# Kernel tuning notes

Hardware: AMD Instinct MI355X
Metric: run time of the kernel (lower is better)

Reference implementation:

```python
import jax, jax.numpy as jnp
import numpy as np

B, T, IN, H, GAT_HEADS, MHA_HEADS, C = 32, 512, 128, 256, 4, 4, 8
OUT = H // GAT_HEADS          # 64, GAT per-head out_features
HD = H // MHA_HEADS           # 64, MHA head dim
ALPHA = 0.2                   # LeakyReLU slope
EPS = 1e-5                    # LayerNorm eps


def setup_inputs() -> dict:
    key = jax.random.key(0)
    ks = iter(jax.random.split(key, 32))
    def rn(shape, scale=0.05):
        return jax.random.normal(next(ks), shape, dtype=jnp.float32) * scale
    return {
        "x": jax.random.normal(next(ks), (B, T, IN), dtype=jnp.float32),
        # GRU layer 0 / 1 (PyTorch gate order r,z,n)
        "gru_W_ih0": rn((3 * H, IN)), "gru_W_hh0": rn((3 * H, H)),
        "gru_b_ih0": rn((3 * H,)), "gru_b_hh0": rn((3 * H,)),
        "gru_W_ih1": rn((3 * H, H)), "gru_W_hh1": rn((3 * H, H)),
        "gru_b_ih1": rn((3 * H,)), "gru_b_hh1": rn((3 * H,)),
        # GAT: per-head W [H,OUT] and additive attention vector a [2*OUT]
        "gat_W": rn((GAT_HEADS, H, OUT)), "gat_a": rn((GAT_HEADS, 2 * OUT)),
        "ln_g": jnp.ones((H,), jnp.float32), "ln_b": jnp.zeros((H,), jnp.float32),
        # MHA packed in-proj (q,k,v) + out-proj
        "mha_in_w": rn((3 * H, H)), "mha_in_b": rn((3 * H,)),
        "mha_out_w": rn((H, H)), "mha_out_b": rn((H,)),
        "fc1_w": rn((H // 2, H)), "fc1_b": rn((H // 2,)),
        "fc2_w": rn((C, H // 2)), "fc2_b": rn((C,)),
    }


def _gru_layer(x, W_ih, W_hh, b_ih, b_hh):
    # x: [B,T,D] -> hidden states [B,T,H]; PyTorch GRU cell math, gates r,z,n
    xp = jnp.einsum('btd,gd->btg', x, W_ih) + b_ih  # precompute input proj [B,T,3H]
    Hh = W_hh.shape[1]
    def step(h, xp_t):
        g = h @ W_hh.T + b_hh
        xr, xz, xn = jnp.split(xp_t, 3, axis=-1)
        hr, hz, hn = jnp.split(g, 3, axis=-1)
        r = jax.nn.sigmoid(xr + hr)
        z = jax.nn.sigmoid(xz + hz)
        n = jnp.tanh(xn + r * hn)
        h_new = (1.0 - z) * n + z * h
        return h_new, h_new
    h0 = jnp.zeros((x.shape[0], Hh), x.dtype)
    _, hs = jax.lax.scan(step, h0, jnp.swapaxes(xp, 0, 1))
    return jnp.swapaxes(hs, 0, 1)


def _gat_head(h_in, W, a):
    # Additive attention decomposed: e_ij = leakyrelu(a1.h_i + a2.h_j)
    # (exactly equals matmul(cat[h_i,h_j], a) without the [B,T,T,2*OUT] tensor)
    h = h_in @ W                       # [B,T,OUT]
    f_src = h @ a[:OUT]                # [B,T]
    f_dst = h @ a[OUT:]                # [B,T]
    e = jax.nn.leaky_relu(f_src[:, :, None] + f_dst[:, None, :], ALPHA)  # [B,T,T]
    attn = jax.nn.softmax(e, axis=-1)  # dropout is identity in eval mode
    return jnp.einsum('bij,bjd->bid', attn, h)


def _layer_norm(x, g, b):
    mu = x.mean(-1, keepdims=True)
    var = jnp.mean((x - mu) ** 2, -1, keepdims=True)
    return (x - mu) * jax.lax.rsqrt(var + EPS) * g + b


def _forward(x, gru_W_ih0, gru_W_hh0, gru_b_ih0, gru_b_hh0,
             gru_W_ih1, gru_W_hh1, gru_b_ih1, gru_b_hh1,
             gat_W, gat_a, ln_g, ln_b,
             mha_in_w, mha_in_b, mha_out_w, mha_out_b,
             fc1_w, fc1_b, fc2_w, fc2_b):
    g = _gru_layer(x, gru_W_ih0, gru_W_hh0, gru_b_ih0, gru_b_hh0)
    g = _gru_layer(g, gru_W_ih1, gru_W_hh1, gru_b_ih1, gru_b_hh1)  # [B,T,H]
    gat_out = jnp.concatenate([_gat_head(g, gat_W[i], gat_a[i]) for i in range(GAT_HEADS)], axis=-1)
    y = _layer_norm(g + gat_out, ln_g, ln_b)
    # Multihead self-attention (4 heads, eval-mode dropout = identity)
    qkv = y @ mha_in_w.T + mha_in_b
    q, k, v = jnp.split(qkv, 3, axis=-1)
    def split_heads(t):
        return t.reshape(t.shape[0], t.shape[1], MHA_HEADS, HD).transpose(0, 2, 1, 3)
    q, k, v = split_heads(q), split_heads(k), split_heads(v)
    scores = jnp.einsum('bhqd,bhkd->bhqk', q, k) / jnp.sqrt(jnp.float32(HD))
    attn = jax.nn.softmax(scores, axis=-1)
    ctx = jnp.einsum('bhqk,bhkd->bhqd', attn, v)
    ctx = ctx.transpose(0, 2, 1, 3).reshape(y.shape[0], y.shape[1], H)
    attn_out = ctx @ mha_out_w.T + mha_out_b
    pooled = attn_out.mean(axis=1)                    # [B,H]
    hid = jax.nn.relu(pooled @ fc1_w.T + fc1_b)
    return hid @ fc2_w.T + fc2_b                      # [B,C]


def reference(x, gru_W_ih0, gru_W_hh0, gru_b_ih0, gru_b_hh0,
              gru_W_ih1, gru_W_hh1, gru_b_ih1, gru_b_hh1,
              gat_W, gat_a, ln_g, ln_b,
              mha_in_w, mha_in_b, mha_out_w, mha_out_b,
              fc1_w, fc1_b, fc2_w, fc2_b):
    return _forward(x, gru_W_ih0, gru_W_hh0, gru_b_ih0, gru_b_hh0,
                    gru_W_ih1, gru_W_hh1, gru_b_ih1, gru_b_hh1,
                    gat_W, gat_a, ln_g, ln_b,
                    mha_in_w, mha_in_b, mha_out_w, mha_out_b,
                    fc1_w, fc1_b, fc2_w, fc2_b)
```

## Files before the change

kernel.cpp:

```cpp
#include <hip/hip_runtime.h>
#include <math.h>

#define BB 32
#define TT 512
#define INF_ 128
#define HH 256
#define H3 768
#define NHEADS 4
#define HDIM 64

typedef _Float16 half_t;
typedef half_t half2_t __attribute__((ext_vector_type(2)));
typedef half_t half4_t __attribute__((ext_vector_type(4)));
typedef half_t f16x8 __attribute__((ext_vector_type(8)));
typedef float f32x4 __attribute__((ext_vector_type(4)));

#if defined(__has_builtin)
#if __has_builtin(__builtin_amdgcn_fdot2)
#define FDOT2(a, b, c) __builtin_amdgcn_fdot2((a), (b), (c), false)
#endif
#endif
#ifndef FDOT2
#define FDOT2(a, b, c) fmaf((float)(a).x, (float)(b).x, fmaf((float)(a).y, (float)(b).y, (c)))
#endif

#define BCH(x) __builtin_bit_cast(half2_t, x)
#define PKH(a, b) __builtin_bit_cast(unsigned, half2_t{(half_t)(a), (half_t)(b)})

__device__ __forceinline__ float wsum(float v) {
#pragma unroll
  for (int o = 32; o > 0; o >>= 1) v += __shfl_xor(v, o, 64);
  return v;
}
__device__ __forceinline__ float wmax(float v) {
#pragma unroll
  for (int o = 32; o > 0; o >>= 1) v = fmaxf(v, __shfl_xor(v, o, 64));
  return v;
}

__global__ void castk(const float* __restrict__ s, half_t* __restrict__ d, int n) {
  int i = (blockIdx.x * 256 + threadIdx.x) * 4;
  if (i < n) {
    float4 v = *(const float4*)(s + i);
    half4_t o = {(half_t)v.x, (half_t)v.y, (half_t)v.z, (half_t)v.w};
    *(half4_t*)(d + i) = o;
  }
}

__global__ __launch_bounds__(256) void gemm_f16(
    const half_t* __restrict__ A, const half_t* __restrict__ B,
    const float* __restrict__ bias, float* __restrict__ C,
    int M, int N, int K) {
  __shared__ __align__(16) half_t As[128][40];
  __shared__ __align__(16) half_t Bs[64][40];
  const int tid = threadIdx.x;
  const int wave = tid >> 6, lane = tid & 63;
  const int m0 = blockIdx.y * 128, n0 = blockIdx.x * 64;
  const int mrow = lane & 15, quad = lane >> 4;
  f32x4 acc00 = {0.f, 0.f, 0.f, 0.f}, acc01 = acc00, acc02 = acc00, acc03 = acc00;
  f32x4 acc10 = acc00, acc11 = acc00, acc12 = acc00, acc13 = acc00;
  for (int k0 = 0; k0 < K; k0 += 32) {
    __syncthreads();
#pragma unroll
    for (int u = 0; u < 2; ++u) {
      int idx = tid + u * 256;
      int row = idx >> 2, seg = idx & 3;
      *(f16x8*)&As[row][seg * 8] =
          *(const f16x8*)&A[(size_t)(m0 + row) * K + k0 + seg * 8];
    }
    {
      int row = tid >> 2, seg = tid & 3;
      *(f16x8*)&Bs[row][seg * 8] =
          *(const f16x8*)&B[(size_t)(n0 + row) * K + k0 + seg * 8];
    }
    __syncthreads();
    f16x8 af0 = *(const f16x8*)&As[wave * 32 + mrow][quad * 8];
    f16x8 af1 = *(const f16x8*)&As[wave * 32 + 16 + mrow][quad * 8];
    f16x8 bf0 = *(const f16x8*)&Bs[mrow][quad * 8];
    f16x8 bf1 = *(const f16x8*)&Bs[16 + mrow][quad * 8];
    f16x8 bf2 = *(const f16x8*)&Bs[32 + mrow][quad * 8];
    f16x8 bf3 = *(const f16x8*)&Bs[48 + mrow][quad * 8];
    acc00 = __builtin_amdgcn_mfma_f32_16x16x32_f16(af0, bf0, acc00, 0, 0, 0);
    acc01 = __builtin_amdgcn_mfma_f32_16x16x32_f16(af0, bf1, acc01, 0, 0, 0);
    acc02 = __builtin_amdgcn_mfma_f32_16x16x32_f16(af0, bf2, acc02, 0, 0, 0);
    acc03 = __builtin_amdgcn_mfma_f32_16x16x32_f16(af0, bf3, acc03, 0, 0, 0);
    acc10 = __builtin_amdgcn_mfma_f32_16x16x32_f16(af1, bf0, acc10, 0, 0, 0);
    acc11 = __builtin_amdgcn_mfma_f32_16x16x32_f16(af1, bf1, acc11, 0, 0, 0);
    acc12 = __builtin_amdgcn_mfma_f32_16x16x32_f16(af1, bf2, acc12, 0, 0, 0);
    acc13 = __builtin_amdgcn_mfma_f32_16x16x32_f16(af1, bf3, acc13, 0, 0, 0);
  }
  float bv0 = bias ? bias[n0 + mrow] : 0.f;
  float bv1 = bias ? bias[n0 + 16 + mrow] : 0.f;
  float bv2 = bias ? bias[n0 + 32 + mrow] : 0.f;
  float bv3 = bias ? bias[n0 + 48 + mrow] : 0.f;
  const int rb = m0 + wave * 32 + quad * 4;
#pragma unroll
  for (int r = 0; r < 4; ++r) {
    float* c0 = C + (size_t)(rb + r) * N + n0;
    c0[mrow] = acc00[r] + bv0;
    c0[16 + mrow] = acc01[r] + bv1;
    c0[32 + mrow] = acc02[r] + bv2;
    c0[48 + mrow] = acc03[r] + bv3;
    float* c1 = C + (size_t)(rb + 16 + r) * N + n0;
    c1[mrow] = acc10[r] + bv0;
    c1[16 + mrow] = acc11[r] + bv1;
    c1[32 + mrow] = acc12[r] + bv2;
    c1[48 + mrow] = acc13[r] + bv3;
  }
}

#define LDW(g, p, a, b, i)                             \
  {                                                    \
    float4 v = (p)[i];                                 \
    g##a = half2_t{(half_t)v.x, (half_t)v.y};          \
    g##b = half2_t{(half_t)v.z, (half_t)v.w};          \
  }
#define LDW28(g, p)                                                        \
  LDW(g, p, 0, 1, 0) LDW(g, p, 2, 3, 1) LDW(g, p, 4, 5, 2)                 \
  LDW(g, p, 6, 7, 3) LDW(g, p, 8, 9, 4) LDW(g, p, 10, 11, 5)               \
  LDW(g, p, 12, 13, 6) LDW(g, p, 14, 15, 7) LDW(g, p, 16, 17, 8)           \
  LDW(g, p, 18, 19, 9) LDW(g, p, 20, 21, 10) LDW(g, p, 22, 23, 11)         \
  LDW(g, p, 24, 25, 12) LDW(g, p, 26, 27, 13) LDW(g, p, 28, 29, 14)        \
  LDW(g, p, 30, 31, 15) LDW(g, p, 32, 33, 16) LDW(g, p, 34, 35, 17)        \
  LDW(g, p, 36, 37, 18) LDW(g, p, 38, 39, 19) LDW(g, p, 40, 41, 20)        \
  LDW(g, p, 42, 43, 21) LDW(g, p, 44, 45, 22) LDW(g, p, 46, 47, 23)        \
  LDW(g, p, 48, 49, 24) LDW(g, p, 50, 51, 25) LDW(g, p, 52, 53, 26)        \
  LDW(g, p, 54, 55, 27)

#define DECL56(g)                                                          \
  half2_t g##0, g##1, g##2, g##3, g##4, g##5, g##6, g##7, g##8, g##9,      \
      g##10, g##11, g##12, g##13, g##14, g##15, g##16, g##17, g##18,       \
      g##19, g##20, g##21, g##22, g##23, g##24, g##25, g##26, g##27,       \
      g##28, g##29, g##30, g##31, g##32, g##33, g##34, g##35, g##36,       \
      g##37, g##38, g##39, g##40, g##41, g##42, g##43, g##44, g##45,       \
      g##46, g##47, g##48, g##49, g##50, g##51, g##52, g##53, g##54, g##55;

#define CHA(c8, a0, a1, a2, a3)                                            \
  {                                                                        \
    float4 v = hp4[c8];                                                    \
    uint4 nv = WSq[((c8)-1) * 512 + tid];                                  \
    half2_t t0 = __builtin_bit_cast(half2_t, v.x);                         \
    half2_t t1 = __builtin_bit_cast(half2_t, v.y);                         \
    half2_t t2 = __builtin_bit_cast(half2_t, v.z);                         \
    half2_t t3 = __builtin_bit_cast(half2_t, v.w);                         \
    ar = FDOT2(wr##a0, t0, ar); az = FDOT2(wz##a0, t0, az); an = FDOT2(BCH(nv.x), t0, an); \
    ar = FDOT2(wr##a1, t1, ar); az = FDOT2(wz##a1, t1, az); an = FDOT2(BCH(nv.y), t1, an); \
    ar = FDOT2(wr##a2, t2, ar); az = FDOT2(wz##a2, t2, az); an = FDOT2(BCH(nv.z), t2, an); \
    ar = FDOT2(wr##a3, t3, ar); az = FDOT2(wz##a3, t3, az); an = FDOT2(BCH(nv.w), t3, an); \
  }

#define CHB(c8)                                                            \
  {                                                                        \
    float4 v = hp4[c8];                                                    \
    uint4 nv = WSq[((c8)-1) * 512 + tid];                                  \
    uint4 rv = WSq[(15 + ((c8)-14)) * 512 + tid];                          \
    uint4 zv = WSq[(17 + ((c8)-14)) * 512 + tid];                          \
    half2_t t0 = __builtin_bit_cast(half2_t, v.x);                         \
    half2_t t1 = __builtin_bit_cast(half2_t, v.y);                         \
    half2_t t2 = __builtin_bit_cast(half2_t, v.z);                         \
    half2_t t3 = __builtin_bit_cast(half2_t, v.w);                         \
    ar = FDOT2(BCH(rv.x), t0, ar); az = FDOT2(BCH(zv.x), t0, az); an = FDOT2(BCH(nv.x), t0, an); \
    ar = FDOT2(BCH(rv.y), t1, ar); az = FDOT2(BCH(zv.y), t1, az); an = FDOT2(BCH(nv.y), t1, an); \
    ar = FDOT2(BCH(rv.z), t2, ar); az = FDOT2(BCH(zv.z), t2, az); an = FDOT2(BCH(nv.z), t2, an); \
    ar = FDOT2(BCH(rv.w), t3, ar); az = FDOT2(BCH(zv.w), t3, az); an = FDOT2(BCH(nv.w), t3, an); \
  }

__device__ __forceinline__ uint4 pk8(const float* p) {
  float4 a = *(const float4*)p;
  float4 b = *(const float4*)(p + 4);
  return uint4{PKH(a.x, a.y), PKH(a.z, a.w), PKH(b.x, b.y), PKH(b.z, b.w)};
}

__global__ __launch_bounds__(512) void gru_layer(
    const float* __restrict__ xp, const float* __restrict__ Whh,
    const float* __restrict__ bhh, float* __restrict__ out,
    half_t* __restrict__ out16) {
  __shared__ __align__(16) uint4 WSq[19 * 512];
  __shared__ __align__(16) half_t hs[2][2][144];
  const int tid = threadIdx.x;
  const int kh = tid & 1, j = tid >> 1;
  const int b = blockIdx.x;
  const bool wf32 = (out != nullptr);
  DECL56(wr)
  DECL56(wz)
  half2_t wn0, wn1, wn2, wn3;
  {
    const float4* pr = (const float4*)(Whh + (size_t)j * HH + kh * 128);
    const float4* pz = (const float4*)(Whh + (size_t)(HH + j) * HH + kh * 128);
    const float4* pn = (const float4*)(Whh + (size_t)(2 * HH + j) * HH + kh * 128);
    LDW28(wr, pr)
    LDW28(wz, pz)
    LDW(wn, pn, 0, 1, 0)
    LDW(wn, pn, 2, 3, 1)
  }
  {
    const float* rowN = Whh + (size_t)(2 * HH + j) * HH + kh * 128;
    const float* rowR = Whh + (size_t)j * HH + kh * 128;
    const float* rowZ = Whh + (size_t)(HH + j) * HH + kh * 128;
#pragma unroll
    for (int sg = 0; sg < 15; ++sg) WSq[sg * 512 + tid] = pk8(rowN + 8 + 8 * sg);
#pragma unroll
    for (int sg = 0; sg < 2; ++sg) WSq[(15 + sg) * 512 + tid] = pk8(rowR + 112 + 8 * sg);
#pragma unroll
    for (int sg = 0; sg < 2; ++sg) WSq[(17 + sg) * 512 + tid] = pk8(rowZ + 112 + 8 * sg);
  }
  const float br = bhh[j], bz = bhh[HH + j], bn = bhh[2 * HH + j];
  for (int i = tid; i < 288; i += 512) ((unsigned*)hs)[i] = 0u;
  __syncthreads();
  float hprev = 0.f;
  const float* xrow = xp + (size_t)b * TT * H3;
  float* orow = out + (size_t)b * TT * HH;
  half_t* orow16 = out16 + (size_t)b * TT * HH;
  for (int t = 0; t < TT; ++t) {
    float xr = xrow[j], xz = xrow[HH + j], xn = xrow[2 * HH + j];
    const float4* hp4 = (const float4*)&hs[t & 1][kh][0];
    float ar = 0.f, az = 0.f, an = 0.f;
    {
      float4 v = hp4[0];
      half2_t t0 = __builtin_bit_cast(half2_t, v.x);
      half2_t t1 = __builtin_bit_cast(half2_t, v.y);
      half2_t t2 = __builtin_bit_cast(half2_t, v.z);
      half2_t t3 = __builtin_bit_cast(half2_t, v.w);
      ar = FDOT2(wr0, t0, ar); az = FDOT2(wz0, t0, az); an = FDOT2(wn0, t0, an);
      ar = FDOT2(wr1, t1, ar); az = FDOT2(wz1, t1, az); an = FDOT2(wn1, t1, an);
      ar = FDOT2(wr2, t2, ar); az = FDOT2(wz2, t2, az); an = FDOT2(wn2, t2, an);
      ar = FDOT2(wr3, t3, ar); az = FDOT2(wz3, t3, az); an = FDOT2(wn3, t3, an);
    }
    CHA(1, 4, 5, 6, 7)
    CHA(2, 8, 9, 10, 11)
    CHA(3, 12, 13, 14, 15)
    CHA(4, 16, 17, 18, 19)
    CHA(5, 20, 21, 22, 23)
    CHA(6, 24, 25, 26, 27)
    CHA(7, 28, 29, 30, 31)
    CHA(8, 32, 33, 34, 35)
    CHA(9, 36, 37, 38, 39)
    CHA(10, 40, 41, 42, 43)
    CHA(11, 44, 45, 46, 47)
    CHA(12, 48, 49, 50, 51)
    CHA(13, 52, 53, 54, 55)
    CHB(14)
    CHB(15)
    ar += __shfl_xor(ar, 1);
    az += __shfl_xor(az, 1);
    an += __shfl_xor(an, 1);
    float rg = 1.f / (1.f + __expf(-(xr + ar + br)));
    float zg = 1.f / (1.f + __expf(-(xz + az + bz)));
    float ng = 2.f / (1.f + __expf(-2.f * (xn + rg * (an + bn)))) - 1.f;
    float hnew = (1.f - zg) * ng + zg * hprev;
    hprev = hnew;
    float hpart = __shfl_xor(hnew, 2);
    if ((tid & 3) == 0) {
      half2_t pk;
      pk.x = (half_t)hnew;
      pk.y = (half_t)hpart;
      *(half2_t*)&hs[(t + 1) & 1][j >> 7][j & 127] = pk;
    }
    if (kh == 0) {
      orow16[j] = (half_t)hnew;
      if (wf32) orow[j] = hnew;
    }
    __syncthreads();
    xrow += H3;
    orow += HH;
    orow16 += HH;
  }
}

__global__ void gat_wt(const float* __restrict__ W, half_t* __restrict__ Wt) {
  int idx = blockIdx.x * 256 + threadIdx.x;
  int col = idx >> 8, k = idx & 255;
  Wt[idx] = (half_t)W[((size_t)((col >> 6) * HH + k)) * HDIM + (col & 63)];
}

__global__ void gat_fsd(const float* __restrict__ hgat, const float* __restrict__ a,
                        float* __restrict__ fsrc, float* __restrict__ fdst) {
  int b = blockIdx.x, hd = blockIdx.y, t = threadIdx.x;
  const float* hp = hgat + ((size_t)(b * TT + t)) * HH + hd * HDIM;
  const float* ap = a + hd * 2 * HDIM;
  float fs = 0.f, fd = 0.f;
#pragma unroll 4
  for (int d = 0; d < HDIM; ++d) {
    float hv = hp[d];
    fs += hv * ap[d];
    fd += hv * ap[HDIM + d];
  }
  fsrc[(b * NHEADS + hd) * TT + t] = fs;
  fdst[(b * NHEADS + hd) * TT + t] = fd;
}

__global__ __launch_bounds__(256) void gat_attn(
    const float* __restrict__ hgat, const float* __restrict__ fsrc,
    const float* __restrict__ fdst, float* __restrict__ out) {
  __shared__ __align__(16) float Ht[128][64];
  __shared__ __align__(16) float fd[128];
  __shared__ __align__(16) float pq[4][128][8];
  const int tid = threadIdx.x, wave = tid >> 6, lane = tid & 63;
  const int hd = blockIdx.y, b = blockIdx.z;
  const int i0 = blockIdx.x * 32 + wave * 8;
  const float* fs = fsrc + (size_t)(b * NHEADS + hd) * TT;
  const float* fdp = fdst + (size_t)(b * NHEADS + hd) * TT;
  float m[8], l[8], acc[8], fi[8];
#pragma unroll
  for (int q = 0; q < 8; ++q) { m[q] = -1e30f; l[q] = 0.f; acc[q] = 0.f; fi[q] = fs[i0 + q]; }
  for (int jt = 0; jt < TT; jt += 128) {
#pragma unroll
    for (int u = 0; u < 8; ++u) {
      int idx = tid + u * 256;
      int jj = idx >> 4, dq = (idx & 15) * 4;
      *(float4*)&Ht[jj][dq] =
          *(const float4*)&hgat[((size_t)(b * TT + jt + jj)) * HH + hd * HDIM + dq];
    }
    if (tid < 128) fd[tid] = fdp[jt + tid];
    __syncthreads();
#pragma unroll
    for (int q = 0; q < 8; ++q) {
      float e0 = fi[q] + fd[lane];      e0 = (e0 > 0.f) ? e0 : 0.2f * e0;
      float e1 = fi[q] + fd[lane + 64]; e1 = (e1 > 0.f) ? e1 : 0.2f * e1;
      float mn = fmaxf(m[q], wmax(fmaxf(e0, e1)));
      float corr = __expf(m[q] - mn);
      float p0 = __expf(e0 - mn), p1 = __expf(e1 - mn);
      l[q] = l[q] * corr + wsum(p0 + p1);
      m[q] = mn;
      acc[q] *= corr;
      pq[wave][lane][q] = p0;
      pq[wave][lane + 64][q] = p1;
    }
#pragma unroll 4
    for (int jj = 0; jj < 128; ++jj) {
      float4 pa = *(const float4*)&pq[wave][jj][0];
      float4 pb = *(const float4*)&pq[wave][jj][4];
      float hv = Ht[jj][lane];
      acc[0] += pa.x * hv; acc[1] += pa.y * hv; acc[2] += pa.z * hv; acc[3] += pa.w * hv;
      acc[4] += pb.x * hv; acc[5] += pb.y * hv; acc[6] += pb.z * hv; acc[7] += pb.w * hv;
    }
    __syncthreads();
  }
#pragma unroll
  for (int q = 0; q < 8; ++q)
    out[((size_t)(b * TT + i0 + q)) * HH + hd * HDIM + lane] = acc[q] / l[q];
}

__global__ __launch_bounds__(256) void ln_res(
    const float* __restrict__ g, const float* __restrict__ gat,
    const float* __restrict__ gamma, const float* __restrict__ beta,
    half_t* __restrict__ y16) {
  int wave = threadIdx.x >> 6, lane = threadIdx.x & 63;
  size_t n = (size_t)blockIdx.x * 4 + wave;
  float4 v = ((const float4*)(g + n * HH))[lane];
  float4 w = ((const float4*)(gat + n * HH))[lane];
  v.x += w.x; v.y += w.y; v.z += w.z; v.w += w.w;
  float mu = wsum(v.x + v.y + v.z + v.w) * (1.f / 256.f);
  float dx = v.x - mu, dy = v.y - mu, dz = v.z - mu, dw = v.w - mu;
  float var = wsum(dx * dx + dy * dy + dz * dz + dw * dw) * (1.f / 256.f);
  float rstd = rsqrtf(var + 1e-5f);
  float4 gm = ((const float4*)gamma)[lane];
  float4 bt = ((const float4*)beta)[lane];
  half4_t o = {(half_t)(dx * rstd * gm.x + bt.x), (half_t)(dy * rstd * gm.y + bt.y),
               (half_t)(dz * rstd * gm.z + bt.z), (half_t)(dw * rstd * gm.w + bt.w)};
  ((half4_t*)(y16 + n * HH))[lane] = o;
}

__global__ __launch_bounds__(256) void mha_attn(const float* __restrict__ qkv,
                                                half_t* __restrict__ ctx16) {
  __shared__ __align__(16) float KV[8320];
  __shared__ __align__(16) float qq[4][64][8];
  __shared__ __align__(16) float pq[4][128][8];
  const int tid = threadIdx.x, wave = tid >> 6, lane = tid & 63;
  const int hd = blockIdx.y, b = blockIdx.z;
  const int i0 = blockIdx.x * 32 + wave * 8;
#pragma unroll
  for (int q = 0; q < 8; ++q)
    qq[wave][lane][q] = qkv[((size_t)(b * TT + i0 + q)) * H3 + hd * HDIM + lane];
  float m[8], l[8], acc[8];
#pragma unroll
  for (int q = 0; q < 8; ++q) { m[q] = -1e30f; l[q] = 0.f; acc[q] = 0.f; }
  for (int jt = 0; jt < TT; jt += 128) {
#pragma unroll
    for (int u = 0; u < 8; ++u) {
      int idx = tid + u * 256;
      int jj = idx >> 4, dq = (idx & 15) * 4;
      float4 kv = *(const float4*)&qkv[((size_t)(b * TT + jt + jj)) * H3 + HH + hd * HDIM + dq];
      KV[(dq + 0) * 130 + jj] = kv.x;
      KV[(dq + 1) * 130 + jj] = kv.y;
      KV[(dq + 2) * 130 + jj] = kv.z;
      KV[(dq + 3) * 130 + jj] = kv.w;
    }
    __syncthreads();
    float e0[8] = {}, e1[8] = {};
#pragma unroll 8
    for (int dd = 0; dd < 64; ++dd) {
      float4 qa = *(const float4*)&qq[wave][dd][0];
      float4 qb = *(const float4*)&qq[wave][dd][4];
      float k0 = KV[dd * 130 + lane], k1 = KV[dd * 130 + 64 + lane];
      e0[0] += qa.x * k0; e0[1] += qa.y * k0; e0[2] += qa.z * k0; e0[3] += qa.w * k0;
      e0[4] += qb.x * k0; e0[5] += qb.y * k0; e0[6] += qb.z * k0; e0[7] += qb.w * k0;
      e1[0] += qa.x * k1; e1[1] += qa.y * k1; e1[2] += qa.z * k1; e1[3] += qa.w * k1;
      e1[4] += qb.x * k1; e1[5] += qb.y * k1; e1[6] += qb.z * k1; e1[7] += qb.w * k1;
    }
    __syncthreads();
#pragma unroll
    for (int u = 0; u < 8; ++u) {
      int idx = tid + u * 256;
      int jj = idx >> 4, dq = (idx & 15) * 4;
      *(float4*)&KV[jj * 64 + dq] =
          *(const float4*)&qkv[((size_t)(b * TT + jt + jj)) * H3 + 2 * HH + hd * HDIM + dq];
    }
#pragma unroll
    for (int q = 0; q < 8; ++q) {
      float s0 = e0[q] * 0.125f, s1 = e1[q] * 0.125f;
      float mn = fmaxf(m[q], wmax(fmaxf(s0, s1)));
      float corr = __expf(m[q] - mn);
      float p0 = __expf(s0 - mn), p1 = __expf(s1 - mn);
      l[q] = l[q] * corr + wsum(p0 + p1);
      m[q] = mn;
      acc[q] *= corr;
      pq[wave][lane][q] = p0;
      pq[wave][lane + 64][q] = p1;
    }
    __syncthreads();
#pragma unroll 4
    for (int jj = 0; jj < 128; ++jj) {
      float4 pa = *(const float4*)&pq[wave][jj][0];
      float4 pb = *(const float4*)&pq[wave][jj][4];
      float hv = KV[jj * 64 + lane];
      acc[0] += pa.x * hv; acc[1] += pa.y * hv; acc[2] += pa.z * hv; acc[3] += pa.w * hv;
      acc[4] += pb.x * hv; acc[5] += pb.y * hv; acc[6] += pb.z * hv; acc[7] += pb.w * hv;
    }
    __syncthreads();
  }
#pragma unroll
  for (int q = 0; q < 8; ++q)
    ctx16[((size_t)(b * TT + i0 + q)) * HH + hd * HDIM + lane] = (half_t)(acc[q] / l[q]);
}

__global__ void mean_pool(const float* __restrict__ x, float* __restrict__ out) {
  int b = blockIdx.x, j = threadIdx.x;
  const float* p = x + (size_t)b * TT * HH + j;
  float s = 0.f;
  for (int t = 0; t < TT; ++t) s += p[(size_t)t * HH];
  out[b * HH + j] = s * (1.f / 512.f);
}

__global__ void fc1_k(const float* __restrict__ pooled, const float* __restrict__ w,
                      const float* __restrict__ bias, float* __restrict__ hid) {
  int b = blockIdx.x, o = threadIdx.x;
  const float* pp = pooled + b * HH;
  const float* wp = w + o * HH;
  float s = 0.f;
#pragma unroll 4
  for (int k = 0; k < HH; ++k) s += pp[k] * wp[k];
  hid[b * 128 + o] = fmaxf(s + bias[o], 0.f);
}

__global__ void fc2_k(const float* __restrict__ hid, const float* __restrict__ w,
                      const float* __restrict__ bias, float* __restrict__ out) {
  int t = threadIdx.x;
  int mm = t >> 3, c = t & 7;
  const float* hp = hid + mm * 128;
  const float* wp = w + c * 128;
  float s = 0.f;
#pragma unroll 4
  for (int k = 0; k < 128; ++k) s += hp[k] * wp[k];
  out[mm * 8 + c] = s + bias[c];
}

extern "C" void kernel_launch(void* const* d_in, const int* in_sizes, int n_in,
                              void* d_out, int out_size, void* d_ws, size_t ws_size,
                              hipStream_t stream) {
  (void)in_sizes; (void)n_in; (void)out_size; (void)ws_size;
  const float* x    = (const float*)d_in[0];
  const float* Wih0 = (const float*)d_in[1];
  const float* Whh0 = (const float*)d_in[2];
  const float* bih0 = (const float*)d_in[3];
  const float* bhh0 = (const float*)d_in[4];
  const float* Wih1 = (const float*)d_in[5];
  const float* Whh1 = (const float*)d_in[6];
  const float* bih1 = (const float*)d_in[7];
  const float* bhh1 = (const float*)d_in[8];
  const float* gatW = (const float*)d_in[9];
  const float* gatA = (const float*)d_in[10];
  const float* lng  = (const float*)d_in[11];
  const float* lnb  = (const float*)d_in[12];
  const float* inw  = (const float*)d_in[13];
  const float* inb  = (const float*)d_in[14];
  const float* outw = (const float*)d_in[15];
  const float* outb = (const float*)d_in[16];
  const float* f1w  = (const float*)d_in[17];
  const float* f1b  = (const float*)d_in[18];
  const float* f2w  = (const float*)d_in[19];
  const float* f2b  = (const float*)d_in[20];
  float* out = (float*)d_out;
  float* ws = (float*)d_ws;

  float* XPA   = ws;
  float* G0    = ws + 12582912;
  float* G1    = G0 + 4194304;
  float* Yb    = G1 + 4194304;
  float* HGAT  = Yb + 4194304;
  float* GATWTf= HGAT + 4194304;
  float* FSRC  = GATWTf + 65536;
  float* FDST  = FSRC + 65536;
  float* POOL  = FDST + 65536;
  float* HIDb  = POOL + 8192;
  float* W16b  = HIDb + 4096;

  half_t* X16     = (half_t*)G1;
  half_t* G0_16   = (half_t*)Yb;
  half_t* G1_16   = (half_t*)(Yb + 2097152);
  half_t* CTX16   = (half_t*)HGAT;
  half_t* Y16     = (half_t*)(HGAT + 2097152);
  half_t* GATWT16 = (half_t*)GATWTf;
  half_t* W16ih0  = (half_t*)W16b;
  half_t* W16ih1  = (half_t*)(W16b + 49152);
  half_t* W16in   = (half_t*)(W16b + 49152 + 98304);
  half_t* W16out  = (half_t*)(W16b + 49152 + 98304 + 98304);

  castk<<<2048, 256, 0, stream>>>(x, X16, 2097152);
  castk<<<96, 256, 0, stream>>>(Wih0, W16ih0, 98304);
  castk<<<192, 256, 0, stream>>>(Wih1, W16ih1, 196608);
  castk<<<192, 256, 0, stream>>>(inw, W16in, 196608);
  castk<<<64, 256, 0, stream>>>(outw, W16out, 65536);
  gat_wt<<<256, 256, 0, stream>>>(gatW, GATWT16);
  gemm_f16<<<dim3(12, 128), 256, 0, stream>>>(X16, W16ih0, bih0, XPA, 16384, 768, 128);
  gru_layer<<<32, 512, 0, stream>>>(XPA, Whh0, bhh0, nullptr, G0_16);
  gemm_f16<<<dim3(12, 128), 256, 0, stream>>>(G0_16, W16ih1, bih1, XPA, 16384, 768, 256);
  gru_layer<<<32, 512, 0, stream>>>(XPA, Whh1, bhh1, G1, G1_16);
  gemm_f16<<<dim3(4, 128), 256, 0, stream>>>(G1_16, GATWT16, nullptr, HGAT, 16384, 256, 256);
  gat_fsd<<<dim3(32, 4), 512, 0, stream>>>(HGAT, gatA, FSRC, FDST);
  gat_attn<<<dim3(16, 4, 32), 256, 0, stream>>>(HGAT, FSRC, FDST, G0);
  ln_res<<<4096, 256, 0, stream>>>(G1, G0, lng, lnb, Y16);
  gemm_f16<<<dim3(12, 128), 256, 0, stream>>>(Y16, W16in, inb, XPA, 16384, 768, 256);
  mha_attn<<<dim3(16, 4, 32), 256, 0, stream>>>(XPA, CTX16);
  gemm_f16<<<dim3(4, 128), 256, 0, stream>>>(CTX16, W16out, outb, Yb, 16384, 256, 256);
  mean_pool<<<32, 256, 0, stream>>>(Yb, POOL);
  fc1_k<<<32, 128, 0, stream>>>(POOL, f1w, f1b, HIDb);
  fc2_k<<<1, 256, 0, stream>>>(HIDb, f2w, f2b, out);
}
```

Measured before the change: 1.933 ms.

## Run GAT and MHA attention on MFMA f16 matrix cores

Rewrites the GAT and MHA attention kernels so their QK^T and PV products use 16x16x32 f16 MFMA instructions instead of scalar FP32 FMAs. K, V and the hidden states are cast to half and staged in shared memory, with V transposed. Each wave now handles 16 query rows, so each block covers 64 queries and the grid shrinks. This aims to cut the ALU-bound cost of the attention kernels, at the price of f16 precision for probabilities and values.

```diff
diff --git a/kernel.cpp b/kernel.cpp
--- a/kernel.cpp
+++ b/kernel.cpp
@@ -45,6 +45,11 @@
     half4_t o = {(half_t)v.x, (half_t)v.y, (half_t)v.z, (half_t)v.w};
     *(half4_t*)(d + i) = o;
   }
+}
+
+__device__ __forceinline__ f16x8 pk16(float4 a, float4 b) {
+  return f16x8{(half_t)a.x, (half_t)a.y, (half_t)a.z, (half_t)a.w,
+               (half_t)b.x, (half_t)b.y, (half_t)b.z, (half_t)b.w};
 }
 
 __global__ __launch_bounds__(256) void gemm_f16(
@@ -292,53 +297,98 @@
 __global__ __launch_bounds__(256) void gat_attn(
     const float* __restrict__ hgat, const float* __restrict__ fsrc,
     const float* __restrict__ fdst, float* __restrict__ out) {
-  __shared__ __align__(16) float Ht[128][64];
+  __shared__ __align__(16) half_t Htt[64][136];
+  __shared__ __align__(16) half_t Ps[4][16][136];
   __shared__ __align__(16) float fd[128];
-  __shared__ __align__(16) float pq[4][128][8];
   const int tid = threadIdx.x, wave = tid >> 6, lane = tid & 63;
+  const int mrow = lane & 15, quad = lane >> 4;
   const int hd = blockIdx.y, b = blockIdx.z;
-  const int i0 = blockIdx.x * 32 + wave * 8;
-  const float* fs = fsrc + (size_t)(b * NHEADS + hd) * TT;
+  const int q0 = blockIdx.x * 64;
+  const float fi = fsrc[(size_t)(b * NHEADS + hd) * TT + q0 + wave * 16 + mrow];
   const float* fdp = fdst + (size_t)(b * NHEADS + hd) * TT;
-  float m[8], l[8], acc[8], fi[8];
-#pragma unroll
-  for (int q = 0; q < 8; ++q) { m[q] = -1e30f; l[q] = 0.f; acc[q] = 0.f; fi[q] = fs[i0 + q]; }
+  float m = -1e30f, l = 0.f;
+  f32x4 o[4];
+#pragma unroll
+  for (int n = 0; n < 4; ++n) o[n] = f32x4{0.f, 0.f, 0.f, 0.f};
   for (int jt = 0; jt < TT; jt += 128) {
 #pragma unroll
-    for (int u = 0; u < 8; ++u) {
+    for (int u = 0; u < 4; ++u) {
       int idx = tid + u * 256;
-      int jj = idx >> 4, dq = (idx & 15) * 4;
-      *(float4*)&Ht[jj][dq] =
-          *(const float4*)&hgat[((size_t)(b * TT + jt + jj)) * HH + hd * HDIM + dq];
-    }
-    if (tid < 128) fd[tid] = fdp[jt + tid];
-    __syncthreads();
-#pragma unroll
-    for (int q = 0; q < 8; ++q) {
-      float e0 = fi[q] + fd[lane];      e0 = (e0 > 0.f) ? e0 : 0.2f * e0;
-      float e1 = fi[q] + fd[lane + 64]; e1 = (e1 > 0.f) ? e1 : 0.2f * e1;
-      float mn = fmaxf(m[q], wmax(fmaxf(e0, e1)));
-      float corr = __expf(m[q] - mn);
-      float p0 = __expf(e0 - mn), p1 = __expf(e1 - mn);
-      l[q] = l[q] * corr + wsum(p0 + p1);
-      m[q] = mn;
-      acc[q] *= corr;
-      pq[wave][lane][q] = p0;
-      pq[wave][lane + 64][q] = p1;
-    }
-#pragma unroll 4
-    for (int jj = 0; jj < 128; ++jj) {
-      float4 pa = *(const float4*)&pq[wave][jj][0];
-      float4 pb = *(const float4*)&pq[wave][jj][4];
-      float hv = Ht[jj][lane];
-      acc[0] += pa.x * hv; acc[1] += pa.y * hv; acc[2] += pa.z * hv; acc[3] += pa.w * hv;
-      acc[4] += pb.x * hv; acc[5] += pb.y * hv; acc[6] += pb.z * hv; acc[7] += pb.w * hv;
-    }
-    __syncthreads();
-  }
-#pragma unroll
-  for (int q = 0; q < 8; ++q)
-    out[((size_t)(b * TT + i0 + q)) * HH + hd * HDIM + lane] = acc[q] / l[q];
+      int j = idx >> 3, s = (idx & 7) * 8;
+      const float* hp = hgat + (size_t)(b * TT + jt + j) * HH + hd * HDIM + s;
+      float4 ha = *(const float4*)hp, hb = *(const float4*)(hp + 4);
+      Htt[s + 0][j] = (half_t)ha.x; Htt[s + 1][j] = (half_t)ha.y;
+      Htt[s + 2][j] = (half_t)ha.z; Htt[s + 3][j] = (half_t)ha.w;
+      Htt[s + 4][j] = (half_t)hb.x; Htt[s + 5][j] = (half_t)hb.y;
+      Htt[s + 6][j] = (half_t)hb.z; Htt[s + 7][j] = (half_t)hb.w;
+    }
+    if (tid < 32) *(float4*)&fd[tid * 4] = *(const float4*)&fdp[jt + tid * 4];
+    __syncthreads();
+    float p[32];
+    float mx = -1e30f;
+#pragma unroll
+    for (int g = 0; g < 8; ++g) {
+      float4 f4 = *(const float4*)&fd[quad * 32 + g * 4];
+      float e0 = fi + f4.x; e0 = (e0 > 0.f) ? e0 : 0.2f * e0;
+      float e1 = fi + f4.y; e1 = (e1 > 0.f) ? e1 : 0.2f * e1;
+      float e2 = fi + f4.z; e2 = (e2 > 0.f) ? e2 : 0.2f * e2;
+      float e3 = fi + f4.w; e3 = (e3 > 0.f) ? e3 : 0.2f * e3;
+      p[g * 4 + 0] = e0; p[g * 4 + 1] = e1; p[g * 4 + 2] = e2; p[g * 4 + 3] = e3;
+      mx = fmaxf(mx, fmaxf(fmaxf(e0, e1), fmaxf(e2, e3)));
+    }
+    mx = fmaxf(mx, __shfl_xor(mx, 16, 64));
+    mx = fmaxf(mx, __shfl_xor(mx, 32, 64));
+    float mn = fmaxf(m, mx);
+    float corr = __expf(m - mn);
+    m = mn;
+    float ls = 0.f;
+#pragma unroll
+    for (int i = 0; i < 32; ++i) { p[i] = __expf(p[i] - mn); ls += p[i]; }
+    ls += __shfl_xor(ls, 16, 64);
+    ls += __shfl_xor(ls, 32, 64);
+    l = l * corr + ls;
+    float cr[4];
+#pragma unroll
+    for (int r = 0; r < 4; ++r) cr[r] = __shfl(corr, quad * 4 + r, 64);
+#pragma unroll
+    for (int n = 0; n < 4; ++n) {
+      o[n][0] *= cr[0]; o[n][1] *= cr[1]; o[n][2] *= cr[2]; o[n][3] *= cr[3];
+    }
+#pragma unroll
+    for (int s8 = 0; s8 < 4; ++s8) {
+      f16x8 pkv = {(half_t)p[s8 * 8 + 0], (half_t)p[s8 * 8 + 1],
+                   (half_t)p[s8 * 8 + 2], (half_t)p[s8 * 8 + 3],
+                   (half_t)p[s8 * 8 + 4], (half_t)p[s8 * 8 + 5],
+                   (half_t)p[s8 * 8 + 6], (half_t)p[s8 * 8 + 7]};
+      *(f16x8*)&Ps[wave][mrow][quad * 32 + s8 * 8] = pkv;
+    }
+    __syncthreads();
+    f16x8 pa0 = *(const f16x8*)&Ps[wave][mrow][0 * 32 + quad * 8];
+    f16x8 pa1 = *(const f16x8*)&Ps[wave][mrow][1 * 32 + quad * 8];
+    f16x8 pa2 = *(const f16x8*)&Ps[wave][mrow][2 * 32 + quad * 8];
+    f16x8 pa3 = *(const f16x8*)&Ps[wave][mrow][3 * 32 + quad * 8];
+#pragma unroll
+    for (int n = 0; n < 4; ++n) {
+      f16x8 vb0 = *(const f16x8*)&Htt[n * 16 + mrow][0 * 32 + quad * 8];
+      f16x8 vb1 = *(const f16x8*)&Htt[n * 16 + mrow][1 * 32 + quad * 8];
+      f16x8 vb2 = *(const f16x8*)&Htt[n * 16 + mrow][2 * 32 + quad * 8];
+      f16x8 vb3 = *(const f16x8*)&Htt[n * 16 + mrow][3 * 32 + quad * 8];
+      o[n] = __builtin_amdgcn_mfma_f32_16x16x32_f16(pa0, vb0, o[n], 0, 0, 0);
+      o[n] = __builtin_amdgcn_mfma_f32_16x16x32_f16(pa1, vb1, o[n], 0, 0, 0);
+      o[n] = __builtin_amdgcn_mfma_f32_16x16x32_f16(pa2, vb2, o[n], 0, 0, 0);
+      o[n] = __builtin_amdgcn_mfma_f32_16x16x32_f16(pa3, vb3, o[n], 0, 0, 0);
+    }
+    __syncthreads();
+  }
+  float lr[4];
+#pragma unroll
+  for (int r = 0; r < 4; ++r) lr[r] = __shfl(l, quad * 4 + r, 64);
+#pragma unroll
+  for (int n = 0; n < 4; ++n)
+#pragma unroll
+    for (int r = 0; r < 4; ++r)
+      out[(size_t)(b * TT + q0 + wave * 16 + quad * 4 + r) * HH + hd * HDIM +
+          n * 16 + mrow] = o[n][r] / lr[r];
 }
 
 __global__ __launch_bounds__(256) void ln_res(
@@ -363,75 +413,125 @@
 
 __global__ __launch_bounds__(256) void mha_attn(const float* __restrict__ qkv,
                                                 half_t* __restrict__ ctx16) {
-  __shared__ __align__(16) float KV[8320];
-  __shared__ __align__(16) float qq[4][64][8];
-  __shared__ __align__(16) float pq[4][128][8];
+  __shared__ __align__(16) half_t Qs[64][72];
+  __shared__ __align__(16) half_t Ks[128][72];
+  __shared__ __align__(16) half_t Vt[64][136];
+  __shared__ __align__(16) half_t Ps[4][16][136];
   const int tid = threadIdx.x, wave = tid >> 6, lane = tid & 63;
+  const int mrow = lane & 15, quad = lane >> 4;
   const int hd = blockIdx.y, b = blockIdx.z;
-  const int i0 = blockIdx.x * 32 + wave * 8;
-#pragma unroll
-  for (int q = 0; q < 8; ++q)
-    qq[wave][lane][q] = qkv[((size_t)(b * TT + i0 + q)) * H3 + hd * HDIM + lane];
-  float m[8], l[8], acc[8];
-#pragma unroll
-  for (int q = 0; q < 8; ++q) { m[q] = -1e30f; l[q] = 0.f; acc[q] = 0.f; }
+  const int q0 = blockIdx.x * 64;
+  {
+    int r = tid >> 2, s = (tid & 3) * 16;
+    const float* src = qkv + (size_t)(b * TT + q0 + r) * H3 + hd * HDIM + s;
+    float4 a = *(const float4*)src, b4 = *(const float4*)(src + 4);
+    float4 c = *(const float4*)(src + 8), d4 = *(const float4*)(src + 12);
+    *(f16x8*)&Qs[r][s] = pk16(a, b4);
+    *(f16x8*)&Qs[r][s + 8] = pk16(c, d4);
+  }
+  __syncthreads();
+  f16x8 qa0 = *(const f16x8*)&Qs[wave * 16 + mrow][quad * 8];
+  f16x8 qa1 = *(const f16x8*)&Qs[wave * 16 + mrow][32 + quad * 8];
+  float m[4] = {-1e30f, -1e30f, -1e30f, -1e30f};
+  float l[4] = {0.f, 0.f, 0.f, 0.f};
+  f32x4 o[4];
+#pragma unroll
+  for (int n = 0; n < 4; ++n) o[n] = f32x4{0.f, 0.f, 0.f, 0.f};
   for (int jt = 0; jt < TT; jt += 128) {
 #pragma unroll
-    for (int u = 0; u < 8; ++u) {
+    for (int u = 0; u < 4; ++u) {
       int idx = tid + u * 256;
-      int jj = idx >> 4, dq = (idx & 15) * 4;
-      float4 kv = *(const float4*)&qkv[((size_t)(b * TT + jt + jj)) * H3 + HH + hd * HDIM + dq];
-      KV[(dq + 0) * 130 + jj] = kv.x;
-      KV[(dq + 1) * 130 + jj] = kv.y;
-      KV[(dq + 2) * 130 + jj] = kv.z;
-      KV[(dq + 3) * 130 + jj] = kv.w;
-    }
-    __syncthreads();
-    float e0[8] = {}, e1[8] = {};
-#pragma unroll 8
-    for (int dd = 0; dd < 64; ++dd) {
-      float4 qa = *(const float4*)&qq[wave][dd][0];
-      float4 qb = *(const float4*)&qq[wave][dd][4];
-      float k0 = KV[dd * 130 + lane], k1 = KV[dd * 130 + 64 + lane];
-      e0[0] += qa.x * k0; e0[1] += qa.y * k0; e0[2] += qa.z * k0; e0[3] += qa.w * k0;
-      e0[4] += qb.x * k0; e0[5] += qb.y * k0; e0[6] += qb.z * k0; e0[7] += qb.w * k0;
-      e1[0] += qa.x * k1; e1[1] += qa.y * k1; e1[2] += qa.z * k1; e1[3] += qa.w * k1;
-      e1[4] += qb.x * k1; e1[5] += qb.y * k1; e1[6] += qb.z * k1; e1[7] += qb.w * k1;
-    }
-    __syncthreads();
-#pragma unroll
-    for (int u = 0; u < 8; ++u) {
-      int idx = tid + u * 256;
-      int jj = idx >> 4, dq = (idx & 15) * 4;
-      *(float4*)&KV[jj * 64 + dq] =
-          *(const float4*)&qkv[((size_t)(b * TT + jt + jj)) * H3 + 2 * HH + hd * HDIM + dq];
-    }
-#pragma unroll
-    for (int q = 0; q < 8; ++q) {
-      float s0 = e0[q] * 0.125f, s1 = e1[q] * 0.125f;
-      float mn = fmaxf(m[q], wmax(fmaxf(s0, s1)));
-      float corr = __expf(m[q] - mn);
-      float p0 = __expf(s0 - mn), p1 = __expf(s1 - mn);
-      l[q] = l[q] * corr + wsum(p0 + p1);
-      m[q] = mn;
-      acc[q] *= corr;
-      pq[wave][lane][q] = p0;
-      pq[wave][lane + 64][q] = p1;
-    }
-    __syncthreads();
-#pragma unroll 4
-    for (int jj = 0; jj < 128; ++jj) {
-      float4 pa = *(const float4*)&pq[wave][jj][0];
-      float4 pb = *(const float4*)&pq[wave][jj][4];
-      float hv = KV[jj * 64 + lane];
-      acc[0] += pa.x * hv; acc[1] += pa.y * hv; acc[2] += pa.z * hv; acc[3] += pa.w * hv;
-      acc[4] += pb.x * hv; acc[5] += pb.y * hv; acc[6] += pb.z * hv; acc[7] += pb.w * hv;
-    }
-    __syncthreads();
-  }
-#pragma unroll
-  for (int q = 0; q < 8; ++q)
-    ctx16[((size_t)(b * TT + i0 + q)) * HH + hd * HDIM + lane] = (half_t)(acc[q] / l[q]);
+      int j = idx >> 3, s = (idx & 7) * 8;
+      const float* kp = qkv + (size_t)(b * TT + jt + j) * H3 + HH + hd * HDIM + s;
+      float4 ka = *(const float4*)kp, kb = *(const float4*)(kp + 4);
+      *(f16x8*)&Ks[j][s] = pk16(ka, kb);
+      const float* vp = kp + HH;
+      float4 va = *(const float4*)vp, vb = *(const float4*)(vp + 4);
+      Vt[s + 0][j] = (half_t)va.x; Vt[s + 1][j] = (half_t)va.y;
+      Vt[s + 2][j] = (half_t)va.z; Vt[s + 3][j] = (half_t)va.w;
+      Vt[s + 4][j] = (half_t)vb.x; Vt[s + 5][j] = (half_t)vb.y;
+      Vt[s + 6][j] = (half_t)vb.z; Vt[s + 7][j] = (half_t)vb.w;
+    }
+    __syncthreads();
+    f32x4 sAcc[8];
+#pragma unroll
+    for (int n = 0; n < 8; ++n) sAcc[n] = f32x4{0.f, 0.f, 0.f, 0.f};
+#pragma unroll
+    for (int n = 0; n < 8; ++n) {
+      f16x8 kb0 = *(const f16x8*)&Ks[n * 16 + mrow][quad * 8];
+      f16x8 kb1 = *(const f16x8*)&Ks[n * 16 + mrow][32 + quad * 8];
+      sAcc[n] = __builtin_amdgcn_mfma_f32_16x16x32_f16(qa0, kb0, sAcc[n], 0, 0, 0);
+      sAcc[n] = __builtin_amdgcn_mfma_f32_16x16x32_f16(qa1, kb1, sAcc[n], 0, 0, 0);
+    }
+    float p[8][4];
+    float mx[4] = {-1e30f, -1e30f, -1e30f, -1e30f};
+#pragma unroll
+    for (int n = 0; n < 8; ++n)
+#pragma unroll
+      for (int r = 0; r < 4; ++r) {
+        float v = sAcc[n][r] * 0.125f;
+        p[n][r] = v;
+        mx[r] = fmaxf(mx[r], v);
+      }
+#pragma unroll
+    for (int off = 8; off > 0; off >>= 1)
+#pragma unroll
+      for (int r = 0; r < 4; ++r) mx[r] = fmaxf(mx[r], __shfl_xor(mx[r], off, 64));
+    float corr[4], ls[4];
+#pragma unroll
+    for (int r = 0; r < 4; ++r) {
+      float mn = fmaxf(m[r], mx[r]);
+      corr[r] = __expf(m[r] - mn);
+      m[r] = mn;
+      ls[r] = 0.f;
+    }
+#pragma unroll
+    for (int n = 0; n < 8; ++n)
+#pragma unroll
+      for (int r = 0; r < 4; ++r) {
+        float e = __expf(p[n][r] - m[r]);
+        p[n][r] = e;
+        ls[r] += e;
+      }
+#pragma unroll
+    for (int off = 8; off > 0; off >>= 1)
+#pragma unroll
+      for (int r = 0; r < 4; ++r) ls[r] += __shfl_xor(ls[r], off, 64);
+#pragma unroll
+    for (int r = 0; r < 4; ++r) l[r] = l[r] * corr[r] + ls[r];
+#pragma unroll
+    for (int n = 0; n < 4; ++n) {
+      o[n][0] *= corr[0]; o[n][1] *= corr[1]; o[n][2] *= corr[2]; o[n][3] *= corr[3];
+    }
+#pragma unroll
+    for (int n = 0; n < 8; ++n)
+#pragma unroll
+      for (int r = 0; r < 4; ++r)
+        Ps[wave][quad * 4 + r][n * 16 + mrow] = (half_t)p[n][r];
+    __syncthreads();
+    f16x8 pa0 = *(const f16x8*)&Ps[wave][mrow][0 * 32 + quad * 8];
+    f16x8 pa1 = *(const f16x8*)&Ps[wave][mrow][1 * 32 + quad * 8];
+    f16x8 pa2 = *(const f16x8*)&Ps[wave][mrow][2 * 32 + quad * 8];
+    f16x8 pa3 = *(const f16x8*)&Ps[wave][mrow][3 * 32 + quad * 8];
+#pragma unroll
+    for (int n = 0; n < 4; ++n) {
+      f16x8 vb0 = *(const f16x8*)&Vt[n * 16 + mrow][0 * 32 + quad * 8];
+      f16x8 vb1 = *(const f16x8*)&Vt[n * 16 + mrow][1 * 32 + quad * 8];
+      f16x8 vb2 = *(const f16x8*)&Vt[n * 16 + mrow][2 * 32 + quad * 8];
+      f16x8 vb3 = *(const f16x8*)&Vt[n * 16 + mrow][3 * 32 + quad * 8];
+      o[n] = __builtin_amdgcn_mfma_f32_16x16x32_f16(pa0, vb0, o[n], 0, 0, 0);
+      o[n] = __builtin_amdgcn_mfma_f32_16x16x32_f16(pa1, vb1, o[n], 0, 0, 0);
+      o[n] = __builtin_amdgcn_mfma_f32_16x16x32_f16(pa2, vb2, o[n], 0, 0, 0);
+      o[n] = __builtin_amdgcn_mfma_f32_16x16x32_f16(pa3, vb3, o[n], 0, 0, 0);
+    }
+    __syncthreads();
+  }
+#pragma unroll
+  for (int n = 0; n < 4; ++n)
+#pragma unroll
+    for (int r = 0; r < 4; ++r)
+      ctx16[(size_t)(b * TT + q0 + wave * 16 + quad * 4 + r) * HH + hd * HDIM +
+            n * 16 + mrow] = (half_t)(o[n][r] / l[r]);
 }
 
 __global__ void mean_pool(const float* __restrict__ x, float* __restrict__ out) {
@@ -528,10 +628,10 @@
   gru_layer<<<32, 512, 0, stream>>>(XPA, Whh1, bhh1, G1, G1_16);
   gemm_f16<<<dim3(4, 128), 256, 0, stream>>>(G1_16, GATWT16, nullptr, HGAT, 16384, 256, 256);
   gat_fsd<<<dim3(32, 4), 512, 0, stream>>>(HGAT, gatA, FSRC, FDST);
-  gat_attn<<<dim3(16, 4, 32), 256, 0, stream>>>(HGAT, FSRC, FDST, G0);
+  gat_attn<<<dim3(8, 4, 32), 256, 0, stream>>>(HGAT, FSRC, FDST, G0);
   ln_res<<<4096, 256, 0, stream>>>(G1, G0, lng, lnb, Y16);
   gemm_f16<<<dim3(12, 128), 256, 0, stream>>>(Y16, W16in, inb, XPA, 16384, 768, 256);
-  mha_attn<<<dim3(16, 4, 32), 256, 0, stream>>>(XPA, CTX16);
+  mha_attn<<<dim3(8, 4, 32), 256, 0, stream>>>(XPA, CTX16);
   gemm_f16<<<dim3(4, 128), 256, 0, stream>>>(CTX16, W16out, outb, Yb, 16384, 256, 256);
   mean_pool<<<32, 256, 0, stream>>>(Yb, POOL);
   fc1_k<<<32, 128, 0, stream>>>(POOL, f1w, f1b, HIDb);
```

Result: faster. 1.678 ms (-13.2%).
